# Performance work log

Hardware: AMD Instinct MI355X
Metric: run time of the kernel (lower is better)

The kernel has to match this reference:

```python
import jax, jax.numpy as jnp
import numpy as np

N, F, D, H = 8192, 128, 128, 2
LEAKY_ALPHA = 0.3  # keras.layers.LeakyReLU default


def setup_inputs() -> dict:
    key = jax.random.key(0)
    ks = jax.random.split(key, 8)
    x = jax.random.normal(ks[0], (N, F), dtype=jnp.float32)
    # sparse-ish binary adjacency with self loops, stored dense (as the module does)
    adj = (jax.random.uniform(ks[1], (N, N)) < 0.01).astype(jnp.float32)
    adj = jnp.clip(adj + jnp.eye(N, dtype=jnp.float32), 0.0, 1.0)
    s = 1.0 / np.sqrt(F)
    Wmap = jax.random.normal(ks[2], (H, F, D), dtype=jnp.float32) * s
    a1_w = jax.random.normal(ks[3], (H, D), dtype=jnp.float32) * (1.0 / np.sqrt(D))
    a2_w = jax.random.normal(ks[4], (H, D), dtype=jnp.float32) * (1.0 / np.sqrt(D))
    a1_b = jnp.zeros((H,), dtype=jnp.float32)
    a2_b = jnp.zeros((H,), dtype=jnp.float32)
    kernel = jax.random.normal(ks[5], (H, F, D), dtype=jnp.float32) * s
    bias = jnp.zeros((H, N, D), dtype=jnp.float32)
    return {"x": x, "adj": adj, "Wmap": Wmap, "a1_w": a1_w, "a1_b": a1_b,
            "a2_w": a2_w, "a2_b": a2_b, "kernel": kernel, "bias": bias}


def reference(x, adj, Wmap, a1_w, a1_b, a2_w, a2_b, kernel, bias):
    # per-head Conv1D(k=1, no bias): node-wise linear map  [H, N, D]
    mapped = jnp.einsum('nf,hfd->hnd', x, Wmap)
    # per-head Conv1D(k=1) scalar scores  [H, N]
    sa1 = jnp.einsum('hnd,hd->hn', mapped, a1_w) + a1_b[:, None]
    sa2 = jnp.einsum('hnd,hd->hn', mapped, a2_w) + a2_b[:, None]
    # additive score masked multiplicatively by adjacency:  [H, N, N]
    w = adj[None, :, :] * sa1[:, :, None] + adj[None, :, :] * sa2[:, None, :]
    w = jnp.where(w >= 0, w, LEAKY_ALPHA * w)
    att = jax.nn.softmax(w, axis=-1)  # softmax over neighbors (incl. zeroed entries, as in source)
    value = jnp.einsum('nf,hfd->hnd', x, kernel)
    out = jnp.einsum('hnm,hmd->hnd', att, value) + bias  # [H, N, D]
    return out.mean(axis=0)  # attn_heads_reduction='average', linear activation
```

## Files before the change

kernel.cpp:

```cpp
#include <hip/hip_runtime.h>

#define NN 8192
#define FF 128
#define DD 128
#define HH 2
#define ALPHA 0.3f
#define MAXNNZ 1024

typedef float v4f __attribute__((ext_vector_type(4)));

__global__ __launch_bounds__(256) void prep_kernel(
    const float* __restrict__ Wmap, const float* __restrict__ a1w,
    const float* __restrict__ a2w, const float* __restrict__ x,
    float* __restrict__ c1, float* __restrict__ c2, float* __restrict__ xsum) {
  int b = blockIdx.x;
  int t = threadIdx.x;
  if (b == 128) {
    int h = t >> 7, f = t & 127;
    const float* wrow = Wmap + ((size_t)h * FF + f) * DD;
    const float* a1 = a1w + h * DD;
    const float* a2 = a2w + h * DD;
    float s1 = 0.f, s2 = 0.f;
    #pragma unroll 8
    for (int d = 0; d < DD; d++) {
      float w = wrow[d];
      s1 += w * a1[d];
      s2 += w * a2[d];
    }
    c1[t] = s1;
    c2[t] = s2;
  } else {
    int f = t & 127, rh = t >> 7;
    const float* xp = x + ((size_t)(b * 64 + rh) * FF) + f;
    float s = 0.f;
    #pragma unroll 8
    for (int r = 0; r < 64; r += 2) s += xp[(size_t)r * FF];
    atomicAdd(&xsum[f], s);
  }
}

__global__ __launch_bounds__(128) void sa_kernel(
    const float* __restrict__ x, const float* __restrict__ c1,
    const float* __restrict__ c2, const float* __restrict__ a1b,
    const float* __restrict__ a2b, float* __restrict__ sa1, float* __restrict__ sa2p) {
  int n = blockIdx.x;
  int f = threadIdx.x;
  float xv = x[(size_t)n * FF + f];
  float p00 = xv * c1[f];
  float p01 = xv * c1[FF + f];
  float p10 = xv * c2[f];
  float p11 = xv * c2[FF + f];
  #pragma unroll
  for (int o = 32; o > 0; o >>= 1) {
    p00 += __shfl_down(p00, o);
    p01 += __shfl_down(p01, o);
    p10 += __shfl_down(p10, o);
    p11 += __shfl_down(p11, o);
  }
  __shared__ float part[2][4];
  int w = f >> 6;
  if ((f & 63) == 0) {
    part[w][0] = p00; part[w][1] = p01; part[w][2] = p10; part[w][3] = p11;
  }
  __syncthreads();
  if (f == 0) {
    sa1[n]      = part[0][0] + part[1][0] + a1b[0];
    sa1[NN + n] = part[0][1] + part[1][1] + a1b[1];
    ((float2*)sa2p)[n] = make_float2(part[0][2] + part[1][2] + a2b[0],
                                     part[0][3] + part[1][3] + a2b[1]);
  }
}

__global__ __launch_bounds__(256) void gat_fused(
    const float* __restrict__ adj, const float* __restrict__ x,
    const float* __restrict__ sa1, const float* __restrict__ sa2p,
    const float* __restrict__ xsum, float* __restrict__ gs) {
  int i = blockIdx.x;
  __shared__ int idxbuf[MAXNNZ];
  __shared__ int cnt;
  __shared__ float esum_sh[8][HH];
  __shared__ v4f vred[HH][8][32];
  int t = threadIdx.x;
  if (t == 0) cnt = 0;
  __syncthreads();

  const v4f* arow = (const v4f*)(adj + (size_t)i * NN);
  #pragma unroll
  for (int q = 0; q < 8; q++) {
    int f4 = q * 256 + t;
    v4f a = __builtin_nontemporal_load(&arow[f4]);
    int j0 = f4 * 4;
    if (a.x != 0.f) { int p = atomicAdd(&cnt, 1); if (p < MAXNNZ) idxbuf[p] = j0; }
    if (a.y != 0.f) { int p = atomicAdd(&cnt, 1); if (p < MAXNNZ) idxbuf[p] = j0 + 1; }
    if (a.z != 0.f) { int p = atomicAdd(&cnt, 1); if (p < MAXNNZ) idxbuf[p] = j0 + 2; }
    if (a.w != 0.f) { int p = atomicAdd(&cnt, 1); if (p < MAXNNZ) idxbuf[p] = j0 + 3; }
  }
  __syncthreads();
  int count = min(cnt, MAXNNZ);

  float s10 = sa1[i];
  float s11 = sa1[NN + i];
  int sub = t & 31;
  int eg  = t >> 5;
  v4f acc0 = {0.f, 0.f, 0.f, 0.f}, acc1 = {0.f, 0.f, 0.f, 0.f};
  float le0 = 0.f, le1 = 0.f;
  const v4f* xb = (const v4f*)x;
  const float2* s2p = (const float2*)sa2p;
  #pragma unroll 2
  for (int k = eg; k < count; k += 8) {
    int j = idxbuf[k];
    float2 s2 = s2p[j];
    v4f xv = xb[(size_t)j * 32 + sub];
    float w0 = s10 + s2.x;
    float w1 = s11 + s2.y;
    w0 = (w0 >= 0.f) ? w0 : ALPHA * w0;
    w1 = (w1 >= 0.f) ? w1 : ALPHA * w1;
    float e0 = __expf(w0) - 1.f;
    float e1 = __expf(w1) - 1.f;
    acc0 += e0 * xv;
    acc1 += e1 * xv;
    le0 += e0;
    le1 += e1;
  }
  vred[0][eg][sub] = acc0;
  vred[1][eg][sub] = acc1;
  if (sub == 0) { esum_sh[eg][0] = le0; esum_sh[eg][1] = le1; }
  __syncthreads();

  if (t < 64) {
    int h = t >> 5, s = t & 31;
    v4f v = vred[h][0][s];
    #pragma unroll
    for (int e = 1; e < 8; e++) v += vred[h][e][s];
    float sume = 0.f;
    #pragma unroll
    for (int e = 0; e < 8; e++) sume += esum_sh[e][h];
    float inv = 0.5f / ((float)NN + sume);
    v4f xs = ((const v4f*)xsum)[s];
    ((v4f*)(gs + (size_t)i * (HH * FF)))[h * 32 + s] = (v + xs) * inv;
  }
}

__global__ __launch_bounds__(256) void out_gemm(
    const float* __restrict__ gs, const float* __restrict__ kern,
    const float* __restrict__ bias, float* __restrict__ out) {
  int row0 = blockIdx.x * 32;
  __shared__ float Bl[64 * 128];
  __shared__ float Al[32 * 132];
  const float4* Bg4 = (const float4*)kern;
  const float4* Ag4 = (const float4*)(gs + (size_t)row0 * 256);
  float4* Bl4 = (float4*)Bl;
  int tid = threadIdx.x;
  int cg = tid & 31;
  int rg = tid >> 5;
  v4f acc[4];
  #pragma unroll
  for (int m = 0; m < 4; m++) acc[m] = (v4f){0.f, 0.f, 0.f, 0.f};

  for (int ka = 0; ka < 2; ka++) {
    __syncthreads();
    #pragma unroll
    for (int q = 0; q < 4; q++) {
      int idx = q * 256 + tid;
      int r = idx >> 5, c4 = idx & 31;
      float4 g = Ag4[r * 64 + ka * 32 + c4];
      *(float4*)&Al[r * 132 + c4 * 4] = g;
    }
    #pragma unroll
    for (int kpi = 0; kpi < 2; kpi++) {
      int kp = ka * 2 + kpi;
      __syncthreads();
      #pragma unroll
      for (int q = 0; q < 8; q++)
        Bl4[q * 256 + tid] = Bg4[kp * 2048 + q * 256 + tid];
      __syncthreads();
      #pragma unroll 4
      for (int kg = 0; kg < 16; kg++) {
        v4f bv0 = *(const v4f*)&Bl[(kg * 4 + 0) * 128 + cg * 4];
        v4f bv1 = *(const v4f*)&Bl[(kg * 4 + 1) * 128 + cg * 4];
        v4f bv2 = *(const v4f*)&Bl[(kg * 4 + 2) * 128 + cg * 4];
        v4f bv3 = *(const v4f*)&Bl[(kg * 4 + 3) * 128 + cg * 4];
        #pragma unroll
        for (int m = 0; m < 4; m++) {
          v4f a4 = *(const v4f*)&Al[(rg + m * 8) * 132 + kpi * 64 + kg * 4];
          acc[m] += a4.x * bv0;
          acc[m] += a4.y * bv1;
          acc[m] += a4.z * bv2;
          acc[m] += a4.w * bv3;
        }
      }
    }
  }

  #pragma unroll
  for (int m = 0; m < 4; m++) {
    int r = row0 + rg + m * 8;
    v4f b0 = *(const v4f*)&bias[((size_t)0 * NN + r) * DD + cg * 4];
    v4f b1 = *(const v4f*)&bias[((size_t)1 * NN + r) * DD + cg * 4];
    v4f o = acc[m] + 0.5f * (b0 + b1);
    *(v4f*)&out[(size_t)r * DD + cg * 4] = o;
  }
}

extern "C" void kernel_launch(void* const* d_in, const int* in_sizes, int n_in,
                              void* d_out, int out_size, void* d_ws, size_t ws_size,
                              hipStream_t stream) {
  const float* x    = (const float*)d_in[0];
  const float* adj  = (const float*)d_in[1];
  const float* Wmap = (const float*)d_in[2];
  const float* a1w  = (const float*)d_in[3];
  const float* a1b  = (const float*)d_in[4];
  const float* a2w  = (const float*)d_in[5];
  const float* a2b  = (const float*)d_in[6];
  const float* kern = (const float*)d_in[7];
  const float* bias = (const float*)d_in[8];
  float* out = (float*)d_out;
  float* ws  = (float*)d_ws;

  float* c1   = ws;
  float* c2   = ws + 256;
  float* sa1  = ws + 512;
  float* sa2p = ws + 16896;
  float* xsum = ws + 33280;
  float* gs   = ws + 33408;

  hipMemsetAsync(xsum, 0, FF * sizeof(float), stream);
  prep_kernel<<<129, 256, 0, stream>>>(Wmap, a1w, a2w, x, c1, c2, xsum);
  sa_kernel<<<NN, 128, 0, stream>>>(x, c1, c2, a1b, a2b, sa1, sa2p);
  gat_fused<<<NN, 256, 0, stream>>>(adj, x, sa1, sa2p, xsum, gs);
  out_gemm<<<NN / 32, 256, 0, stream>>>(gs, kern, bias, out);
}
```

Baseline: 414.2 us.

## Fuse prep and score kernels, prefetch neighbor gathers, halve GEMM row tile

```diff
diff --git a/kernel.cpp b/kernel.cpp
--- a/kernel.cpp
+++ b/kernel.cpp
@@ -9,65 +9,67 @@
 
 typedef float v4f __attribute__((ext_vector_type(4)));
 
-__global__ __launch_bounds__(256) void prep_kernel(
+__global__ __launch_bounds__(256) void prep_sa(
     const float* __restrict__ Wmap, const float* __restrict__ a1w,
-    const float* __restrict__ a2w, const float* __restrict__ x,
-    float* __restrict__ c1, float* __restrict__ c2, float* __restrict__ xsum) {
-  int b = blockIdx.x;
-  int t = threadIdx.x;
-  if (b == 128) {
+    const float* __restrict__ a2w, const float* __restrict__ a1b,
+    const float* __restrict__ a2b, const float* __restrict__ x,
+    float* __restrict__ sa1, float* __restrict__ sa2p, float* __restrict__ xsum) {
+  __shared__ float c1s[2 * FF], c2s[2 * FF];
+  __shared__ float xsp[4][FF];
+  int b = blockIdx.x, t = threadIdx.x;
+
+  {
     int h = t >> 7, f = t & 127;
-    const float* wrow = Wmap + ((size_t)h * FF + f) * DD;
-    const float* a1 = a1w + h * DD;
-    const float* a2 = a2w + h * DD;
-    float s1 = 0.f, s2 = 0.f;
+    const v4f* wrow = (const v4f*)(Wmap + ((size_t)h * FF + f) * DD);
+    const v4f* a1 = (const v4f*)(a1w + h * DD);
+    const v4f* a2 = (const v4f*)(a2w + h * DD);
+    v4f s1 = {0.f, 0.f, 0.f, 0.f}, s2 = {0.f, 0.f, 0.f, 0.f};
     #pragma unroll 8
-    for (int d = 0; d < DD; d++) {
-      float w = wrow[d];
-      s1 += w * a1[d];
-      s2 += w * a2[d];
-    }
-    c1[t] = s1;
-    c2[t] = s2;
-  } else {
-    int f = t & 127, rh = t >> 7;
-    const float* xp = x + ((size_t)(b * 64 + rh) * FF) + f;
-    float s = 0.f;
-    #pragma unroll 8
-    for (int r = 0; r < 64; r += 2) s += xp[(size_t)r * FF];
-    atomicAdd(&xsum[f], s);
-  }
-}
-
-__global__ __launch_bounds__(128) void sa_kernel(
-    const float* __restrict__ x, const float* __restrict__ c1,
-    const float* __restrict__ c2, const float* __restrict__ a1b,
-    const float* __restrict__ a2b, float* __restrict__ sa1, float* __restrict__ sa2p) {
-  int n = blockIdx.x;
-  int f = threadIdx.x;
-  float xv = x[(size_t)n * FF + f];
-  float p00 = xv * c1[f];
-  float p01 = xv * c1[FF + f];
-  float p10 = xv * c2[f];
-  float p11 = xv * c2[FF + f];
-  #pragma unroll
-  for (int o = 32; o > 0; o >>= 1) {
-    p00 += __shfl_down(p00, o);
-    p01 += __shfl_down(p01, o);
-    p10 += __shfl_down(p10, o);
-    p11 += __shfl_down(p11, o);
-  }
-  __shared__ float part[2][4];
-  int w = f >> 6;
-  if ((f & 63) == 0) {
-    part[w][0] = p00; part[w][1] = p01; part[w][2] = p10; part[w][3] = p11;
-  }
-  __syncthreads();
-  if (f == 0) {
-    sa1[n]      = part[0][0] + part[1][0] + a1b[0];
-    sa1[NN + n] = part[0][1] + part[1][1] + a1b[1];
-    ((float2*)sa2p)[n] = make_float2(part[0][2] + part[1][2] + a2b[0],
-                                     part[0][3] + part[1][3] + a2b[1]);
+    for (int d4 = 0; d4 < DD / 4; d4++) {
+      v4f wv = wrow[d4];
+      s1 += wv * a1[d4];
+      s2 += wv * a2[d4];
+    }
+    c1s[t] = s1.x + s1.y + s1.z + s1.w;
+    c2s[t] = s2.x + s2.y + s2.z + s2.w;
+  }
+  __syncthreads();
+
+  int w = t >> 6, l = t & 63;
+  float c10 = c1s[2 * l],      c11 = c1s[2 * l + 1];
+  float c1h0 = c1s[FF + 2 * l], c1h1 = c1s[FF + 2 * l + 1];
+  float c20 = c2s[2 * l],      c21 = c2s[2 * l + 1];
+  float c2h0 = c2s[FF + 2 * l], c2h1 = c2s[FF + 2 * l + 1];
+  float b10 = a1b[0], b11 = a1b[1], b20 = a2b[0], b21 = a2b[1];
+  float xa0 = 0.f, xa1 = 0.f;
+  for (int rr = 0; rr < 16; rr++) {
+    int n = b * 64 + w * 16 + rr;
+    float2 xv = ((const float2*)(x + (size_t)n * FF))[l];
+    xa0 += xv.x;
+    xa1 += xv.y;
+    float p00 = xv.x * c10 + xv.y * c11;
+    float p01 = xv.x * c1h0 + xv.y * c1h1;
+    float p10 = xv.x * c20 + xv.y * c21;
+    float p11 = xv.x * c2h0 + xv.y * c2h1;
+    #pragma unroll
+    for (int o = 32; o > 0; o >>= 1) {
+      p00 += __shfl_down(p00, o);
+      p01 += __shfl_down(p01, o);
+      p10 += __shfl_down(p10, o);
+      p11 += __shfl_down(p11, o);
+    }
+    if (l == 0) {
+      sa1[n]      = p00 + b10;
+      sa1[NN + n] = p01 + b11;
+      ((float2*)sa2p)[n] = make_float2(p10 + b20, p11 + b21);
+    }
+  }
+  xsp[w][2 * l]     = xa0;
+  xsp[w][2 * l + 1] = xa1;
+  __syncthreads();
+  if (t < FF) {
+    float s = xsp[0][t] + xsp[1][t] + xsp[2][t] + xsp[3][t];
+    atomicAdd(&xsum[t], s);
   }
 }
 
@@ -106,11 +108,15 @@
   float le0 = 0.f, le1 = 0.f;
   const v4f* xb = (const v4f*)x;
   const float2* s2p = (const float2*)sa2p;
-  #pragma unroll 2
+
+  int j = (eg < count) ? idxbuf[eg] : 0;
+  float2 s2 = s2p[j];
+  v4f xv = xb[(size_t)j * 32 + sub];
   for (int k = eg; k < count; k += 8) {
-    int j = idxbuf[k];
-    float2 s2 = s2p[j];
-    v4f xv = xb[(size_t)j * 32 + sub];
+    int kn = k + 8;
+    int jn = (kn < count) ? idxbuf[kn] : 0;
+    float2 s2n = s2p[jn];
+    v4f xvn = xb[(size_t)jn * 32 + sub];
     float w0 = s10 + s2.x;
     float w1 = s11 + s2.y;
     w0 = (w0 >= 0.f) ? w0 : ALPHA * w0;
@@ -121,6 +127,7 @@
     acc1 += e1 * xv;
     le0 += e0;
     le1 += e1;
+    j = jn; s2 = s2n; xv = xvn;
   }
   vred[0][eg][sub] = acc0;
   vred[1][eg][sub] = acc1;
@@ -144,23 +151,23 @@
 __global__ __launch_bounds__(256) void out_gemm(
     const float* __restrict__ gs, const float* __restrict__ kern,
     const float* __restrict__ bias, float* __restrict__ out) {
-  int row0 = blockIdx.x * 32;
+  int row0 = blockIdx.x * 16;
   __shared__ float Bl[64 * 128];
-  __shared__ float Al[32 * 132];
+  __shared__ float Al[16 * 132];
   const float4* Bg4 = (const float4*)kern;
   const float4* Ag4 = (const float4*)(gs + (size_t)row0 * 256);
   float4* Bl4 = (float4*)Bl;
   int tid = threadIdx.x;
   int cg = tid & 31;
   int rg = tid >> 5;
-  v4f acc[4];
-  #pragma unroll
-  for (int m = 0; m < 4; m++) acc[m] = (v4f){0.f, 0.f, 0.f, 0.f};
+  v4f acc[2];
+  acc[0] = (v4f){0.f, 0.f, 0.f, 0.f};
+  acc[1] = (v4f){0.f, 0.f, 0.f, 0.f};
 
   for (int ka = 0; ka < 2; ka++) {
     __syncthreads();
     #pragma unroll
-    for (int q = 0; q < 4; q++) {
+    for (int q = 0; q < 2; q++) {
       int idx = q * 256 + tid;
       int r = idx >> 5, c4 = idx & 31;
       float4 g = Ag4[r * 64 + ka * 32 + c4];
@@ -181,7 +188,7 @@
         v4f bv2 = *(const v4f*)&Bl[(kg * 4 + 2) * 128 + cg * 4];
         v4f bv3 = *(const v4f*)&Bl[(kg * 4 + 3) * 128 + cg * 4];
         #pragma unroll
-        for (int m = 0; m < 4; m++) {
+        for (int m = 0; m < 2; m++) {
           v4f a4 = *(const v4f*)&Al[(rg + m * 8) * 132 + kpi * 64 + kg * 4];
           acc[m] += a4.x * bv0;
           acc[m] += a4.y * bv1;
@@ -193,7 +200,7 @@
   }
 
   #pragma unroll
-  for (int m = 0; m < 4; m++) {
+  for (int m = 0; m < 2; m++) {
     int r = row0 + rg + m * 8;
     v4f b0 = *(const v4f*)&bias[((size_t)0 * NN + r) * DD + cg * 4];
     v4f b1 = *(const v4f*)&bias[((size_t)1 * NN + r) * DD + cg * 4];
@@ -217,16 +224,13 @@
   float* out = (float*)d_out;
   float* ws  = (float*)d_ws;
 
-  float* c1   = ws;
-  float* c2   = ws + 256;
-  float* sa1  = ws + 512;
-  float* sa2p = ws + 16896;
-  float* xsum = ws + 33280;
-  float* gs   = ws + 33408;
+  float* sa1  = ws;
+  float* sa2p = ws + 16384;
+  float* xsum = ws + 32768;
+  float* gs   = ws + 32896;
 
   hipMemsetAsync(xsum, 0, FF * sizeof(float), stream);
-  prep_kernel<<<129, 256, 0, stream>>>(Wmap, a1w, a2w, x, c1, c2, xsum);
-  sa_kernel<<<NN, 128, 0, stream>>>(x, c1, c2, a1b, a2b, sa1, sa2p);
+  prep_sa<<<128, 256, 0, stream>>>(Wmap, a1w, a2w, a1b, a2b, x, sa1, sa2p, xsum);
   gat_fused<<<NN, 256, 0, stream>>>(adj, x, sa1, sa2p, xsum, gs);
-  out_gemm<<<NN / 32, 256, 0, stream>>>(gs, kern, bias, out);
-}
+  out_gemm<<<NN / 16, 256, 0, stream>>>(gs, kern, bias, out);
+}
```

After: 419.6 us. No clear change (+1.3%).
